# Kernel optimization log

Measured on AMD Instinct MI355X. Metric: run time of the kernel, lower is better.

Reference implementation:

```python
import jax, jax.numpy as jnp
import numpy as np

LAMDA = 0.5

def setup_inputs() -> dict:
    key = jax.random.key(0)
    k1, k2 = jax.random.split(key)
    X_set = jax.random.normal(k1, (8192, 128), dtype=jnp.float32)
    Y_set = jax.random.randint(k2, (8192,), 0, 100, dtype=jnp.int64)
    return {"X_set": X_set, "Y_set": Y_set}

def _pairwise_euclidean(X):
    # X: [N, D] -> D: [N, N] euclidean distances (torch.cdist p=2)
    sq_norms = jnp.sum(X * X, axis=1)  # [N]
    sq = sq_norms[:, None] + sq_norms[None, :] - 2.0 * (X @ X.T)  # [N, N]
    sq = jnp.maximum(sq, 0.0)
    # safe sqrt (zero diagonal) to stay grad-safe under jit
    pos = sq > 0.0
    return jnp.where(pos, jnp.sqrt(jnp.where(pos, sq, 1.0)), 0.0)

def reference(X_set, Y_set):
    X = X_set.reshape(X_set.shape[0], -1)
    D = _pairwise_euclidean(X)  # [N, N]
    same = Y_set[:, None] == Y_set[None, :]  # [N, N] bool
    # Class loop in original == sum of within-class distances (incl. zero diag)
    # minus lamda * sum over all ordered cross-class pairs (each unordered
    # cross pair is counted once for each of its two classes -> full mask).
    pos_sum = jnp.sum(jnp.where(same, D, 0.0))
    neg_sum = jnp.sum(jnp.where(same, 0.0, D))
    return pos_sum - LAMDA * neg_sum
```

## Files before the change

### kernel.cpp

```cpp
#include <hip/hip_runtime.h>

#define N_ROWS 8192
#define DIM    128
#define BM     128
#define NBLK   (N_ROWS / BM)
#define NTRI   (NBLK * (NBLK + 1) / 2)

#define BLOB_PER_RB   65536
#define BLOB_PER_PH   16384

typedef _Float16 half8 __attribute__((ext_vector_type(8)));
typedef float    f32x16 __attribute__((ext_vector_type(16)));

typedef const __attribute__((address_space(1))) unsigned int glb_uint;
typedef __attribute__((address_space(3))) unsigned int lds_uint;

__device__ inline void gload_lds16(const void* g, void* l)
{
    __builtin_amdgcn_global_load_lds((glb_uint*)(uintptr_t)g,
                                     (lds_uint*)(uintptr_t)l, 16, 0, 0);
}

__global__ __launch_bounds__(256)
void prep_tiled(const float* __restrict__ X, char* __restrict__ blob,
                float* __restrict__ norms)
{
    const int t   = blockIdx.x * 256 + threadIdx.x;
    const int gg  = t & 3;
    const int p   = (t >> 2) & 3;
    const int row = t >> 4;

    const float4* src = (const float4*)(X + (size_t)row * DIM + p * 32 + gg * 8);
    const float4 v0 = src[0], v1 = src[1];
    const float xs[8] = {v0.x, v0.y, v0.z, v0.w, v1.x, v1.y, v1.z, v1.w};

    half8 h, l;
    float ns = 0.0f;
    #pragma unroll
    for (int i = 0; i < 8; ++i) {
        const float x = xs[i];
        const _Float16 hh = (_Float16)x;
        h[i] = hh;
        l[i] = (_Float16)(x - (float)hh);
        ns = fmaf(x, x, ns);
    }

    const int rb = row >> 7, r = row & 127;
    char* base = blob + (size_t)rb * BLOB_PER_RB + p * BLOB_PER_PH + r * 128;
    *(half8*)(base + (((gg    ) ^ (r & 7)) << 4)) = h;
    *(half8*)(base + (((gg + 4) ^ (r & 7)) << 4)) = l;

    #pragma unroll
    for (int off = 1; off <= 8; off <<= 1) ns += __shfl_xor(ns, off);
    if ((t & 15) == 0) norms[row] = ns;
}

__global__ __launch_bounds__(256)
void pairsum_mfma(const char* __restrict__ blob, const float* __restrict__ norms,
                  const int* __restrict__ Y, double* __restrict__ gsum)
{
    const int kb = blockIdx.x;
    int bi = (int)((129.0f - sqrtf(fmaf(-8.0f, (float)kb, 129.0f * 129.0f))) * 0.5f);
    while ((bi + 1) * (129 - (bi + 1)) / 2 <= kb) ++bi;
    while (bi * (129 - bi) / 2 > kb) --bi;
    const int bj = bi + (kb - bi * (129 - bi) / 2);
    const int i0 = bi * BM, j0 = bj * BM;

    const int tid  = threadIdx.x;
    const int lane = tid & 63;
    const int w    = tid >> 6;
    const int wy   = w >> 1;
    const int wx   = w & 1;
    const int lr   = lane & 31;
    const int lh   = lane >> 5;

    __shared__ __align__(16) char tile[65536];
    __shared__ float nI[BM], nJ[BM];
    __shared__ int   yI[BM], yJ[BM];
    __shared__ double wsum[4];

    if (tid < BM) { nI[tid] = norms[i0 + tid]; yI[tid] = Y[i0 + tid]; }
    else { const int r = tid & (BM - 1); nJ[r] = norms[j0 + r]; yJ[r] = Y[j0 + r]; }
    __syncthreads();

    const char* Ablob = blob + (size_t)bi * BLOB_PER_RB;
    const char* Bblob = blob + (size_t)bj * BLOB_PER_RB;

    auto STAGE = [&](int p, int s) {
        const char* gA = Ablob + p * BLOB_PER_PH + tid * 16;
        const char* gB = Bblob + p * BLOB_PER_PH + tid * 16;
        char* lA = tile + s * 32768 + tid * 16;
        #pragma unroll
        for (int q = 0; q < 4; ++q) {
            gload_lds16(gA + q * 4096, lA + q * 4096);
            gload_lds16(gB + q * 4096, lA + 16384 + q * 4096);
        }
    };

    f32x16 acc[2][2];
    #pragma unroll
    for (int m = 0; m < 2; ++m)
        #pragma unroll
        for (int n = 0; n < 2; ++n)
            #pragma unroll
            for (int r = 0; r < 16; ++r)
                acc[m][n][r] = 0.0f;

    STAGE(0, 0);
    STAGE(1, 1);

    #pragma unroll
    for (int p = 0; p < 4; ++p) {
        if (p < 3) asm volatile("s_waitcnt vmcnt(8)" ::: "memory");
        else       asm volatile("s_waitcnt vmcnt(0)" ::: "memory");
        __builtin_amdgcn_s_barrier();
        __builtin_amdgcn_sched_barrier(0);

        const char* Ab = tile + ((p & 1) ? 32768 : 0);
        const char* Bb = Ab + 16384;
        #pragma unroll
        for (int ks = 0; ks < 2; ++ks) {
            const int g = ks * 2 + lh;
            half8 ah[2], al[2], bh[2], bl[2];
            #pragma unroll
            for (int m = 0; m < 2; ++m) {
                const int ar = wy * 64 + m * 32 + lr;
                const int ao = ar * 128 + (((g ^ (ar & 7))) << 4);
                ah[m] = *(const half8*)(Ab + ao);
                al[m] = *(const half8*)(Ab + (ao ^ 64));
                const int br = wx * 64 + m * 32 + lr;
                const int bo = br * 128 + (((g ^ (br & 7))) << 4);
                bh[m] = *(const half8*)(Bb + bo);
                bl[m] = *(const half8*)(Bb + (bo ^ 64));
            }
            #pragma unroll
            for (int m = 0; m < 2; ++m)
                #pragma unroll
                for (int n = 0; n < 2; ++n) {
                    acc[m][n] = __builtin_amdgcn_mfma_f32_32x32x16_f16(ah[m], bh[n], acc[m][n], 0, 0, 0);
                    acc[m][n] = __builtin_amdgcn_mfma_f32_32x32x16_f16(ah[m], bl[n], acc[m][n], 0, 0, 0);
                    acc[m][n] = __builtin_amdgcn_mfma_f32_32x32x16_f16(al[m], bh[n], acc[m][n], 0, 0, 0);
                }
        }

        __builtin_amdgcn_sched_barrier(0);
        __builtin_amdgcn_s_barrier();
        if (p + 2 < 4) STAGE(p + 2, p & 1);
    }

    float s = 0.0f;
    float nJv[2]; int yJv[2];
    #pragma unroll
    for (int n = 0; n < 2; ++n) {
        const int lj = wx * 64 + n * 32 + lr;
        nJv[n] = nJ[lj]; yJv[n] = yJ[lj];
    }
    #pragma unroll
    for (int m = 0; m < 2; ++m) {
        #pragma unroll
        for (int r = 0; r < 16; ++r) {
            const int rowin = (r & 3) + 8 * (r >> 2) + 4 * lh;
            const int li = wy * 64 + m * 32 + rowin;
            const float ni = nI[li];
            const int   yi = yI[li];
            const int   gi = i0 + li;
            #pragma unroll
            for (int n = 0; n < 2; ++n) {
                const int gj = j0 + wx * 64 + n * 32 + lr;
                float sq = fmaf(-2.0f, acc[m][n][r], ni + nJv[n]);
                sq = fmaxf(sq, 0.0f);
                const float d = __builtin_amdgcn_sqrtf(sq);
                if (gi < gj) s = fmaf((yi == yJv[n]) ? 1.0f : -0.5f, d, s);
            }
        }
    }

    #pragma unroll
    for (int off = 32; off > 0; off >>= 1) s += __shfl_down(s, off);
    if (lane == 0) wsum[w] = (double)s;
    __syncthreads();
    if (tid == 0) atomicAdd(gsum, wsum[0] + wsum[1] + wsum[2] + wsum[3]);
}

__global__ void finalize_kernel(const double* __restrict__ gsum, float* __restrict__ out)
{
    out[0] = (float)(2.0 * gsum[0]);
}

#define LDSPAD 4
#define LDB (BM + LDSPAD)
__global__ __launch_bounds__(256)
void pairsum_valu(const float* __restrict__ X, const int* __restrict__ Y,
                  double* __restrict__ gsum)
{
    const int bj = blockIdx.x, bi = blockIdx.y;
    if (bi > bj) return;
    const int tid = threadIdx.x;
    const int i0 = bi * BM, j0 = bj * BM;
    __shared__ float As[32][LDB], Bs[32][LDB];
    __shared__ float nI[BM], nJ[BM];
    __shared__ int yI[BM], yJ[BM];
    __shared__ double wsum[4];
    {
        const int r = tid & (BM - 1);
        const bool isJ = tid >= BM;
        const int row = (isJ ? j0 : i0) + r;
        const float4* p = (const float4*)(X + (size_t)row * DIM);
        float s = 0.f;
        #pragma unroll
        for (int q = 0; q < DIM / 4; ++q) {
            float4 v = p[q];
            s = fmaf(v.x, v.x, s); s = fmaf(v.y, v.y, s);
            s = fmaf(v.z, v.z, s); s = fmaf(v.w, v.w, s);
        }
        if (isJ) { nJ[r] = s; yJ[r] = Y[row]; }
        else     { nI[r] = s; yI[r] = Y[row]; }
    }
    float dot[8][8];
    #pragma unroll
    for (int m = 0; m < 8; ++m)
        #pragma unroll
        for (int n = 0; n < 8; ++n) dot[m][n] = 0.f;
    const int tx = tid & 15, ty = tid >> 4;
    for (int kc = 0; kc < DIM; kc += 32) {
        __syncthreads();
        #pragma unroll
        for (int p = 0; p < 4; ++p) {
            const int s2 = p * 256 + tid;
            const int row = s2 >> 3, kg = s2 & 7;
            const float4 va = *(const float4*)(X + (size_t)(i0 + row) * DIM + kc + kg * 4);
            const float4 vb = *(const float4*)(X + (size_t)(j0 + row) * DIM + kc + kg * 4);
            As[kg*4+0][row] = va.x; As[kg*4+1][row] = va.y;
            As[kg*4+2][row] = va.z; As[kg*4+3][row] = va.w;
            Bs[kg*4+0][row] = vb.x; Bs[kg*4+1][row] = vb.y;
            Bs[kg*4+2][row] = vb.z; Bs[kg*4+3][row] = vb.w;
        }
        __syncthreads();
        #pragma unroll
        for (int k = 0; k < 32; ++k) {
            float a[8], b[8];
            *(float4*)&a[0] = *(const float4*)&As[k][ty*8];
            *(float4*)&a[4] = *(const float4*)&As[k][ty*8+4];
            *(float4*)&b[0] = *(const float4*)&Bs[k][tx*8];
            *(float4*)&b[4] = *(const float4*)&Bs[k][tx*8+4];
            #pragma unroll
            for (int m = 0; m < 8; ++m)
                #pragma unroll
                for (int n = 0; n < 8; ++n)
                    dot[m][n] = fmaf(a[m], b[n], dot[m][n]);
        }
    }
    float s = 0.f;
    const int ib = ty * 8, jb = tx * 8;
    #pragma unroll
    for (int m = 0; m < 8; ++m) {
        const int gi = i0 + ib + m;
        const float ni = nI[ib + m];
        const int yi = yI[ib + m];
        #pragma unroll
        for (int n = 0; n < 8; ++n) {
            const int gj = j0 + jb + n;
            float sq = fmaf(-2.f, dot[m][n], ni + nJ[jb + n]);
            sq = fmaxf(sq, 0.f);
            const float d = __builtin_amdgcn_sqrtf(sq);
            if (gi < gj) s = fmaf((yi == yJ[jb + n]) ? 1.0f : -0.5f, d, s);
        }
    }
    #pragma unroll
    for (int off = 32; off > 0; off >>= 1) s += __shfl_down(s, off);
    const int lane = tid & 63, wid = tid >> 6;
    if (lane == 0) wsum[wid] = (double)s;
    __syncthreads();
    if (tid == 0) atomicAdd(gsum, wsum[0] + wsum[1] + wsum[2] + wsum[3]);
}

extern "C" void kernel_launch(void* const* d_in, const int* in_sizes, int n_in,
                              void* d_out, int out_size, void* d_ws, size_t ws_size,
                              hipStream_t stream)
{
    const float* X = (const float*)d_in[0];
    const int*   Y = (const int*)d_in[1];
    float* out = (float*)d_out;

    const size_t OFF_BLOB = 64;
    const size_t OFF_NORM = OFF_BLOB + (size_t)NBLK * BLOB_PER_RB;
    const size_t REQ      = OFF_NORM + (size_t)N_ROWS * 4;

    double* gsum = (double*)d_ws;
    hipMemsetAsync(d_ws, 0, sizeof(double), stream);

    if (ws_size >= REQ) {
        char*  blob  = (char*)d_ws + OFF_BLOB;
        float* norms = (float*)((char*)d_ws + OFF_NORM);
        prep_tiled<<<(N_ROWS * 16) / 256, 256, 0, stream>>>(X, blob, norms);
        pairsum_mfma<<<NTRI, 256, 0, stream>>>(blob, norms, Y, gsum);
    } else {
        dim3 grid(NBLK, NBLK);
        pairsum_valu<<<grid, 256, 0, stream>>>(X, Y, gsum);
    }
    finalize_kernel<<<1, 1, 0, stream>>>(gsum, out);
}
```

Baseline: 105.5 us.

## Single-buffer LDS tile with fragment-ordered blob layout to raise occupancy

The prep kernel now writes the fp16 hi/lo split in an MFMA-fragment-ordered layout, so each lane reads its operand with a contiguous lane*16 offset and needs no XOR swizzle. The main kernel drops the LDS double buffer, halving LDS to 32 KB, and sets launch bounds to 4 blocks per CU so more blocks can be resident at once. The price is that global loads are no longer prefetched ahead of compute: each phase waits on vmcnt(0) before computing. Latency hiding therefore has to come from other resident blocks rather than from software pipelining.

```diff
diff --git a/kernel.cpp b/kernel.cpp
--- a/kernel.cpp
+++ b/kernel.cpp
@@ -25,12 +25,12 @@
 void prep_tiled(const float* __restrict__ X, char* __restrict__ blob,
                 float* __restrict__ norms)
 {
-    const int t   = blockIdx.x * 256 + threadIdx.x;
-    const int gg  = t & 3;
-    const int p   = (t >> 2) & 3;
-    const int row = t >> 4;
-
-    const float4* src = (const float4*)(X + (size_t)row * DIM + p * 32 + gg * 8);
+    const int t    = blockIdx.x * 256 + threadIdx.x;
+    const int ksub = t & 3;
+    const int p    = (t >> 2) & 3;
+    const int row  = t >> 4;
+
+    const float4* src = (const float4*)(X + (size_t)row * DIM + p * 32 + ksub * 8);
     const float4 v0 = src[0], v1 = src[1];
     const float xs[8] = {v0.x, v0.y, v0.z, v0.w, v1.x, v1.y, v1.z, v1.w};
 
@@ -45,17 +45,22 @@
         ns = fmaf(x, x, ns);
     }
 
-    const int rb = row >> 7, r = row & 127;
-    char* base = blob + (size_t)rb * BLOB_PER_RB + p * BLOB_PER_PH + r * 128;
-    *(half8*)(base + (((gg    ) ^ (r & 7)) << 4)) = h;
-    *(half8*)(base + (((gg + 4) ^ (r & 7)) << 4)) = l;
+    const int rb   = row >> 7;
+    const int r    = row & 127;
+    const int g32  = r >> 5;
+    const int q    = ksub >> 1;
+    const int slot = (r & 31) + (ksub & 1) * 32;
+    char* base = blob + (size_t)rb * BLOB_PER_RB + p * BLOB_PER_PH
+               + g32 * 4096 + q * 1024 + slot * 16;
+    *(half8*)(base)        = h;
+    *(half8*)(base + 2048) = l;
 
     #pragma unroll
     for (int off = 1; off <= 8; off <<= 1) ns += __shfl_xor(ns, off);
     if ((t & 15) == 0) norms[row] = ns;
 }
 
-__global__ __launch_bounds__(256)
+__global__ __launch_bounds__(256, 4)
 void pairsum_mfma(const char* __restrict__ blob, const float* __restrict__ norms,
                   const int* __restrict__ Y, double* __restrict__ gsum)
 {
@@ -74,7 +79,7 @@
     const int lr   = lane & 31;
     const int lh   = lane >> 5;
 
-    __shared__ __align__(16) char tile[65536];
+    __shared__ __align__(16) char tile[32768];
     __shared__ float nI[BM], nJ[BM];
     __shared__ int   yI[BM], yJ[BM];
     __shared__ double wsum[4];
@@ -83,19 +88,8 @@
     else { const int r = tid & (BM - 1); nJ[r] = norms[j0 + r]; yJ[r] = Y[j0 + r]; }
     __syncthreads();
 
-    const char* Ablob = blob + (size_t)bi * BLOB_PER_RB;
-    const char* Bblob = blob + (size_t)bj * BLOB_PER_RB;
-
-    auto STAGE = [&](int p, int s) {
-        const char* gA = Ablob + p * BLOB_PER_PH + tid * 16;
-        const char* gB = Bblob + p * BLOB_PER_PH + tid * 16;
-        char* lA = tile + s * 32768 + tid * 16;
-        #pragma unroll
-        for (int q = 0; q < 4; ++q) {
-            gload_lds16(gA + q * 4096, lA + q * 4096);
-            gload_lds16(gB + q * 4096, lA + 16384 + q * 4096);
-        }
-    };
+    const char* Apan = blob + (size_t)bi * BLOB_PER_RB;
+    const char* Bpan = blob + (size_t)bj * BLOB_PER_RB;
 
     f32x16 acc[2][2];
     #pragma unroll
@@ -106,32 +100,28 @@
             for (int r = 0; r < 16; ++r)
                 acc[m][n][r] = 0.0f;
 
-    STAGE(0, 0);
-    STAGE(1, 1);
-
-    #pragma unroll
     for (int p = 0; p < 4; ++p) {
-        if (p < 3) asm volatile("s_waitcnt vmcnt(8)" ::: "memory");
-        else       asm volatile("s_waitcnt vmcnt(0)" ::: "memory");
+        #pragma unroll
+        for (int r = 0; r < 4; ++r) {
+            gload_lds16(Apan + p * BLOB_PER_PH + r * 4096 + tid * 16,
+                        tile + r * 4096 + tid * 16);
+            gload_lds16(Bpan + p * BLOB_PER_PH + r * 4096 + tid * 16,
+                        tile + 16384 + r * 4096 + tid * 16);
+        }
+        asm volatile("s_waitcnt vmcnt(0)" ::: "memory");
         __builtin_amdgcn_s_barrier();
-        __builtin_amdgcn_sched_barrier(0);
-
-        const char* Ab = tile + ((p & 1) ? 32768 : 0);
-        const char* Bb = Ab + 16384;
-        #pragma unroll
-        for (int ks = 0; ks < 2; ++ks) {
-            const int g = ks * 2 + lh;
+
+        #pragma unroll
+        for (int q = 0; q < 2; ++q) {
             half8 ah[2], al[2], bh[2], bl[2];
             #pragma unroll
             for (int m = 0; m < 2; ++m) {
-                const int ar = wy * 64 + m * 32 + lr;
-                const int ao = ar * 128 + (((g ^ (ar & 7))) << 4);
-                ah[m] = *(const half8*)(Ab + ao);
-                al[m] = *(const half8*)(Ab + (ao ^ 64));
-                const int br = wx * 64 + m * 32 + lr;
-                const int bo = br * 128 + (((g ^ (br & 7))) << 4);
-                bh[m] = *(const half8*)(Bb + bo);
-                bl[m] = *(const half8*)(Bb + (bo ^ 64));
+                const int ga = (wy * 2 + m) * 4096 + q * 1024 + lane * 16;
+                ah[m] = *(const half8*)(tile + ga);
+                al[m] = *(const half8*)(tile + ga + 2048);
+                const int gb = 16384 + (wx * 2 + m) * 4096 + q * 1024 + lane * 16;
+                bh[m] = *(const half8*)(tile + gb);
+                bl[m] = *(const half8*)(tile + gb + 2048);
             }
             #pragma unroll
             for (int m = 0; m < 2; ++m)
@@ -142,10 +132,7 @@
                     acc[m][n] = __builtin_amdgcn_mfma_f32_32x32x16_f16(al[m], bh[n], acc[m][n], 0, 0, 0);
                 }
         }
-
-        __builtin_amdgcn_sched_barrier(0);
         __builtin_amdgcn_s_barrier();
-        if (p + 2 < 4) STAGE(p + 2, p & 1);
     }
 
     float s = 0.0f;
```

After: 109.2 us. +3.6%, slower.
